# Optimization experiments

Hardware: AMD Instinct MI355X
Metric: run time of the kernel (lower is better)

Reference implementation:

```python
import jax, jax.numpy as jnp
import numpy as np

B, DIM, COND, HID = 500000, 3, 64, 128
IN = DIM + COND + 1  # z + context + time feature


def setup_inputs() -> dict:
    key = jax.random.key(0)
    ks = jax.random.split(key, 8)
    s_in = 1.0 / np.sqrt(IN)
    s_h = 1.0 / np.sqrt(HID)
    return {
        "t": jnp.float32(0.5),
        "z": jax.random.normal(ks[0], (B, DIM), jnp.float32),
        "logp": jnp.zeros((B, 1), jnp.float32),
        "context": jax.random.normal(ks[1], (B, COND), jnp.float32),
        "eps": jax.random.normal(ks[2], (B, DIM), jnp.float32),
        "W_in": jax.random.normal(ks[3], (IN, HID), jnp.float32) * s_in,
        "b_in": jnp.zeros((HID,), jnp.float32),
        "W_h1": jax.random.normal(ks[4], (HID, HID), jnp.float32) * s_h,
        "b_h1": jnp.zeros((HID,), jnp.float32),
        "W_h2": jax.random.normal(ks[5], (HID, HID), jnp.float32) * s_h,
        "b_h2": jnp.zeros((HID,), jnp.float32),
        "W_out": jax.random.normal(ks[6], (HID, DIM), jnp.float32) * s_h,
        "b_out": jnp.zeros((DIM,), jnp.float32),
        "out_scale": jnp.float32(1.0),
    }


def reference(t, z, logp, context, eps, W_in, b_in, W_h1, b_h1, W_h2, b_h2,
              W_out, b_out, out_scale):
    t_feat = jnp.full((z.shape[0], 1), t, dtype=z.dtype)

    def vel(zz):
        inp = jnp.concatenate([zz, context, t_feat], axis=1)  # (B, IN)
        h = jnp.tanh(inp @ W_in + b_in)
        h = jnp.tanh(h @ W_h1 + b_h1)
        h = jnp.tanh(h @ W_h2 + b_h2)
        return (h @ W_out + b_out) * out_scale  # (B, DIM)

    # Hutchinson trace: tr(df/dz) ~= eps^T (d/dz)(f . eps) via vjp with cotangent eps
    f, vjp_fn = jax.vjp(vel, z)
    (gz,) = vjp_fn(eps)
    neg_div = -jnp.sum(gz * eps, axis=1, keepdims=True)  # (B, 1)
    return f, neg_div
```

## Files before the change

kernel.cpp:

```cpp
#include <hip/hip_runtime.h>


#define B_N    500000
#define NT32   15625
#define GRID   256
#define NSTR   (GRID * 8)

#define L_WFIN   0
#define L_WF1    8704
#define L_WF2    25600
#define L_WB2    42496
#define L_WB1    59392
#define L_WOUTP  76288
#define L_WOUTT  76800
#define L_WIN3   77196
#define L_F16END 77592
#define N_BIAS   384
#define PREP_N   (L_F16END + N_BIAS)
#define BIAS_BYTE   155184
#define OUTST_BYTE  156720
#define LDS_BYTES   159792
#define COPY16      9795

typedef _Float16 f16x4 __attribute__((ext_vector_type(4)));
typedef float    f32x4 __attribute__((ext_vector_type(4)));

union U4 { f16x4 v; _Float16 e[4]; uint2 d; };

static __device__ inline f16x4 lds_a4(const _Float16* p) {
    U4 u; u.d = *reinterpret_cast<const uint2*>(p); return u.v;
}

#define MFMA(a, b, c) __builtin_amdgcn_mfma_f32_16x16x16f16((a), (b), (c), 0, 0, 0)

static __device__ inline float ftanh(float x) {
    float e = __expf(2.f * x);
    return 1.f - 2.f * __builtin_amdgcn_rcpf(e + 1.f);
}

__global__ void prep_kernel(const float* __restrict__ W_in,
                            const float* __restrict__ W_h1,
                            const float* __restrict__ W_h2,
                            const float* __restrict__ W_out,
                            const float* __restrict__ b_in,
                            const float* __restrict__ b_h1,
                            const float* __restrict__ b_h2,
                            _Float16* __restrict__ ws) {
    int i = blockIdx.x * 256 + threadIdx.x;
    if (i >= PREP_N) return;
    if (i >= L_F16END) {
        int bi = i - L_F16END;
        float* bp = reinterpret_cast<float*>(ws + L_F16END);
        bp[bi] = (bi < 128) ? b_in[bi] : (bi < 256) ? b_h1[bi - 128]
                                                    : b_h2[bi - 256];
        return;
    }
    float v = 0.f;
    if (i < L_WF1) {
        int n = i / 68, k = i - n * 68;
        if      (k < 64)  v = W_in[(3 + k) * 128 + n];
        else if (k < 67)  v = W_in[(k - 64) * 128 + n];
        else              v = W_in[67 * 128 + n];
    } else if (i < L_WF2) {
        int j = i - L_WF1; int n = j / 132, a = j - n * 132;
        if (a < 128) v = W_h1[a * 128 + n];
    } else if (i < L_WB2) {
        int j = i - L_WF2; int n = j / 132, a = j - n * 132;
        if (a < 128) v = W_h2[a * 128 + n];
    } else if (i < L_WB1) {
        int j = i - L_WB2; int r = j / 132, b = j - r * 132;
        if (b < 128) v = W_h2[r * 128 + b];
    } else if (i < L_WOUTP) {
        int j = i - L_WB1; int r = j / 132, b = j - r * 132;
        if (b < 128) v = W_h1[r * 128 + b];
    } else if (i < L_WOUTT) {
        int j = i - L_WOUTP; int n = j >> 2, k = j & 3;
        if (k < 3) v = W_out[n * 3 + k];
    } else if (i < L_WIN3) {
        int j = i - L_WOUTT; int d = j / 132, n = j - d * 132;
        if (n < 128) v = W_out[n * 3 + d];
    } else {
        int j = i - L_WIN3; int d = j / 132, a = j - d * 132;
        if (a < 128) v = W_in[d * 128 + a];
    }
    ws[i] = (_Float16)v;
}

__global__ __launch_bounds__(512, 1) void fused_kernel(
        const float* __restrict__ t_p,  const float* __restrict__ z,
        const float* __restrict__ ctx,  const float* __restrict__ eps,
        const float* __restrict__ b_out, const float* __restrict__ os_p,
        const _Float16* __restrict__ ws, float* __restrict__ out) {
    extern __shared__ _Float16 smem[];
    const int tid  = threadIdx.x;
    const int wave = tid >> 6;
    const int lane = tid & 63;
    const int l15  = lane & 15;
    const int q    = lane >> 4;

    {
        const uint4* src = reinterpret_cast<const uint4*>(ws);
        uint4* dst = reinterpret_cast<uint4*>(smem);
        for (int i = tid; i < COPY16; i += 512) dst[i] = src[i];
    }
    __syncthreads();

    const _Float16* WFIN  = smem + L_WFIN;
    const _Float16* WF1   = smem + L_WF1;
    const _Float16* WF2   = smem + L_WF2;
    const _Float16* WB2   = smem + L_WB2;
    const _Float16* WB1   = smem + L_WB1;
    const _Float16* WOUTP = smem + L_WOUTP;
    const _Float16* WOUTT = smem + L_WOUTT;
    const _Float16* WIN3  = smem + L_WIN3;
    const float* biasf =
        reinterpret_cast<const float*>(reinterpret_cast<char*>(smem) + BIAS_BYTE);
    float* outst =
        reinterpret_cast<float*>(reinterpret_cast<char*>(smem) + OUTST_BYTE)
        + wave * 96;

    const float tval = t_p[0];
    const float os   = os_p[0];
    const float bo0 = b_out[0], bo1 = b_out[1], bo2 = b_out[2];
    float* out_f  = out;
    float* out_nd = out + (size_t)B_N * 3;

    const f32x4 zero4 = {0.f, 0.f, 0.f, 0.f};

    for (int t = blockIdx.x * 8 + wave; t < NT32; t += NSTR) {
        const int gb = t * 32;

        U4 epsb[2];
        float ee[2][3];
        #pragma unroll
        for (int c = 0; c < 2; ++c) {
            epsb[c].d.x = 0u; epsb[c].d.y = 0u;
            ee[c][0] = ee[c][1] = ee[c][2] = 0.f;
            if (q == 0) {
                const float* ep = eps + (size_t)(gb + 16 * c + l15) * 3;
                ee[c][0] = ep[0]; ee[c][1] = ep[1]; ee[c][2] = ep[2];
                epsb[c].e[0] = (_Float16)ee[c][0];
                epsb[c].e[1] = (_Float16)ee[c][1];
                epsb[c].e[2] = (_Float16)ee[c][2];
            }
        }

        f32x4 acc[8][2];
        #pragma unroll
        for (int m = 0; m < 8; ++m) { acc[m][0] = zero4; acc[m][1] = zero4; }

        #pragma unroll
        for (int kk = 0; kk < 4; ++kk) {
            U4 b[2];
            #pragma unroll
            for (int c = 0; c < 2; ++c) {
                const float4 cv = *reinterpret_cast<const float4*>(
                    ctx + (size_t)(gb + 16 * c + l15) * 64 + kk * 16 + 4 * q);
                b[c].e[0] = (_Float16)cv.x; b[c].e[1] = (_Float16)cv.y;
                b[c].e[2] = (_Float16)cv.z; b[c].e[3] = (_Float16)cv.w;
            }
            #pragma unroll
            for (int m = 0; m < 8; ++m) {
                f16x4 a = lds_a4(WFIN + (16 * m + l15) * 68 + kk * 16 + 4 * q);
                acc[m][0] = MFMA(a, b[0].v, acc[m][0]);
                acc[m][1] = MFMA(a, b[1].v, acc[m][1]);
            }
        }
        {
            U4 b[2];
            #pragma unroll
            for (int c = 0; c < 2; ++c) {
                b[c].d.x = 0u; b[c].d.y = 0u;
                if (q == 0) {
                    const float* zp = z + (size_t)(gb + 16 * c + l15) * 3;
                    b[c].e[0] = (_Float16)zp[0]; b[c].e[1] = (_Float16)zp[1];
                    b[c].e[2] = (_Float16)zp[2]; b[c].e[3] = (_Float16)tval;
                }
            }
            #pragma unroll
            for (int m = 0; m < 8; ++m) {
                f16x4 a = lds_a4(WFIN + (16 * m + l15) * 68 + 64 + 4 * q);
                acc[m][0] = MFMA(a, b[0].v, acc[m][0]);
                acc[m][1] = MFMA(a, b[1].v, acc[m][1]);
            }
        }
        U4 h1p[8][2];
        #pragma unroll
        for (int m = 0; m < 8; ++m) {
            const float4 bb = *reinterpret_cast<const float4*>(
                biasf + 0 + 16 * m + 4 * q);
            #pragma unroll
            for (int c = 0; c < 2; ++c) {
                h1p[m][c].e[0] = (_Float16)ftanh(acc[m][c][0] + bb.x);
                h1p[m][c].e[1] = (_Float16)ftanh(acc[m][c][1] + bb.y);
                h1p[m][c].e[2] = (_Float16)ftanh(acc[m][c][2] + bb.z);
                h1p[m][c].e[3] = (_Float16)ftanh(acc[m][c][3] + bb.w);
            }
        }

        #pragma unroll
        for (int m = 0; m < 8; ++m) { acc[m][0] = zero4; acc[m][1] = zero4; }
        #pragma unroll
        for (int kk = 0; kk < 8; ++kk) {
            #pragma unroll
            for (int m = 0; m < 8; ++m) {
                f16x4 a = lds_a4(WF1 + (16 * m + l15) * 132 + 16 * kk + 4 * q);
                acc[m][0] = MFMA(a, h1p[kk][0].v, acc[m][0]);
                acc[m][1] = MFMA(a, h1p[kk][1].v, acc[m][1]);
            }
        }
        U4 h2p[8][2];
        #pragma unroll
        for (int m = 0; m < 8; ++m) {
            const float4 bb = *reinterpret_cast<const float4*>(
                biasf + 128 + 16 * m + 4 * q);
            #pragma unroll
            for (int c = 0; c < 2; ++c) {
                h2p[m][c].e[0] = (_Float16)ftanh(acc[m][c][0] + bb.x);
                h2p[m][c].e[1] = (_Float16)ftanh(acc[m][c][1] + bb.y);
                h2p[m][c].e[2] = (_Float16)ftanh(acc[m][c][2] + bb.z);
                h2p[m][c].e[3] = (_Float16)ftanh(acc[m][c][3] + bb.w);
            }
        }

        #pragma unroll
        for (int m = 0; m < 8; ++m) { acc[m][0] = zero4; acc[m][1] = zero4; }
        #pragma unroll
        for (int kk = 0; kk < 8; ++kk) {
            #pragma unroll
            for (int m = 0; m < 8; ++m) {
                f16x4 a = lds_a4(WF2 + (16 * m + l15) * 132 + 16 * kk + 4 * q);
                acc[m][0] = MFMA(a, h2p[kk][0].v, acc[m][0]);
                acc[m][1] = MFMA(a, h2p[kk][1].v, acc[m][1]);
            }
        }
        U4 h3p[8][2], u3p[8][2];
        #pragma unroll
        for (int m = 0; m < 8; ++m) {
            const float4 bb = *reinterpret_cast<const float4*>(
                biasf + 256 + 16 * m + 4 * q);
            f16x4 a3 = lds_a4(WOUTP + (16 * m + l15) * 4 + 4 * q);
            #pragma unroll
            for (int c = 0; c < 2; ++c) {
                f32x4 up = MFMA(a3, epsb[c].v, zero4);
                #pragma unroll
                for (int i = 0; i < 4; ++i) {
                    float bi = (i == 0) ? bb.x : (i == 1) ? bb.y
                              : (i == 2) ? bb.z : bb.w;
                    float h = ftanh(acc[m][c][i] + bi);
                    h3p[m][c].e[i] = (_Float16)h;
                    u3p[m][c].e[i] = (_Float16)(os * up[i] * (1.f - h * h));
                }
            }
        }

        {
            f32x4 f0 = zero4, f1 = zero4;
            #pragma unroll
            for (int kk = 0; kk < 8; ++kk) {
                f16x4 a = lds_a4(WOUTT + l15 * 132 + 16 * kk + 4 * q);
                f0 = MFMA(a, h3p[kk][0].v, f0);
                f1 = MFMA(a, h3p[kk][1].v, f1);
            }
            if (q == 0) {
                outst[(0 * 16 + l15) * 3 + 0] = (f0[0] + bo0) * os;
                outst[(0 * 16 + l15) * 3 + 1] = (f0[1] + bo1) * os;
                outst[(0 * 16 + l15) * 3 + 2] = (f0[2] + bo2) * os;
                outst[(1 * 16 + l15) * 3 + 0] = (f1[0] + bo0) * os;
                outst[(1 * 16 + l15) * 3 + 1] = (f1[1] + bo1) * os;
                outst[(1 * 16 + l15) * 3 + 2] = (f1[2] + bo2) * os;
            }
        }

        #pragma unroll
        for (int m = 0; m < 8; ++m) { acc[m][0] = zero4; acc[m][1] = zero4; }
        #pragma unroll
        for (int kk = 0; kk < 8; ++kk) {
            #pragma unroll
            for (int m = 0; m < 8; ++m) {
                f16x4 a = lds_a4(WB2 + (16 * m + l15) * 132 + 16 * kk + 4 * q);
                acc[m][0] = MFMA(a, u3p[kk][0].v, acc[m][0]);
                acc[m][1] = MFMA(a, u3p[kk][1].v, acc[m][1]);
            }
        }
        #pragma unroll
        for (int m = 0; m < 8; ++m)
            #pragma unroll
            for (int c = 0; c < 2; ++c) {
                U4 u2;
                #pragma unroll
                for (int i = 0; i < 4; ++i) {
                    float h = (float)h2p[m][c].e[i];
                    u2.e[i] = (_Float16)(acc[m][c][i] * (1.f - h * h));
                }
                h2p[m][c] = u2;
            }

        #pragma unroll
        for (int m = 0; m < 8; ++m) { acc[m][0] = zero4; acc[m][1] = zero4; }
        #pragma unroll
        for (int kk = 0; kk < 8; ++kk) {
            #pragma unroll
            for (int m = 0; m < 8; ++m) {
                f16x4 a = lds_a4(WB1 + (16 * m + l15) * 132 + 16 * kk + 4 * q);
                acc[m][0] = MFMA(a, h2p[kk][0].v, acc[m][0]);
                acc[m][1] = MFMA(a, h2p[kk][1].v, acc[m][1]);
            }
        }
        #pragma unroll
        for (int m = 0; m < 8; ++m)
            #pragma unroll
            for (int c = 0; c < 2; ++c) {
                U4 u1;
                #pragma unroll
                for (int i = 0; i < 4; ++i) {
                    float h = (float)h1p[m][c].e[i];
                    u1.e[i] = (_Float16)(acc[m][c][i] * (1.f - h * h));
                }
                h1p[m][c] = u1;
            }

        {
            f32x4 g0 = zero4, g1 = zero4;
            #pragma unroll
            for (int kk = 0; kk < 8; ++kk) {
                f16x4 a = lds_a4(WIN3 + l15 * 132 + 16 * kk + 4 * q);
                g0 = MFMA(a, h1p[kk][0].v, g0);
                g1 = MFMA(a, h1p[kk][1].v, g1);
            }
            if (q == 0) {
                out_nd[gb + l15] =
                    -(g0[0] * ee[0][0] + g0[1] * ee[0][1] + g0[2] * ee[0][2]);
                out_nd[gb + 16 + l15] =
                    -(g1[0] * ee[1][0] + g1[1] * ee[1][1] + g1[2] * ee[1][2]);
            }
        }

        if (lane < 24) {
            float4 v = *reinterpret_cast<const float4*>(outst + lane * 4);
            *reinterpret_cast<float4*>(out_f + (size_t)gb * 3 + lane * 4) = v;
        }
    }
}

extern "C" void kernel_launch(void* const* d_in, const int* in_sizes, int n_in,
                              void* d_out, int out_size, void* d_ws, size_t ws_size,
                              hipStream_t stream) {
    const float* t_p   = (const float*)d_in[0];
    const float* z     = (const float*)d_in[1];
    const float* ctx   = (const float*)d_in[3];
    const float* eps   = (const float*)d_in[4];
    const float* W_in  = (const float*)d_in[5];
    const float* b_in  = (const float*)d_in[6];
    const float* W_h1  = (const float*)d_in[7];
    const float* b_h1  = (const float*)d_in[8];
    const float* W_h2  = (const float*)d_in[9];
    const float* b_h2  = (const float*)d_in[10];
    const float* W_out = (const float*)d_in[11];
    const float* b_out = (const float*)d_in[12];
    const float* os_p  = (const float*)d_in[13];
    _Float16* ws = (_Float16*)d_ws;
    float* out = (float*)d_out;

    static bool attr_set = false;
    if (!attr_set) {
        (void)hipFuncSetAttribute((const void*)fused_kernel,
                                  hipFuncAttributeMaxDynamicSharedMemorySize,
                                  LDS_BYTES);
        attr_set = true;
    }

    prep_kernel<<<(PREP_N + 255) / 256, 256, 0, stream>>>(
        W_in, W_h1, W_h2, W_out, b_in, b_h1, b_h2, ws);
    fused_kernel<<<GRID, 512, LDS_BYTES, stream>>>(
        t_p, z, ctx, eps, b_out, os_p, ws, out);
}
```

Baseline: 334.8 us.

## Switch to 16x16x32 MFMA with permuted weights and raise to 12 waves per block

After: 356.0 us. 1.06x slower.

```diff
diff --git a/kernel.cpp b/kernel.cpp
--- a/kernel.cpp
+++ b/kernel.cpp
@@ -4,7 +4,8 @@
 #define B_N    500000
 #define NT32   15625
 #define GRID   256
-#define NSTR   (GRID * 8)
+#define WPB    12
+#define NSTR   (GRID * WPB)
 
 #define L_WFIN   0
 #define L_WF1    8704
@@ -19,23 +20,36 @@
 #define PREP_N   (L_F16END + N_BIAS)
 #define BIAS_BYTE   155184
 #define OUTST_BYTE  156720
-#define LDS_BYTES   159792
+#define LDS_BYTES   161328
 #define COPY16      9795
 
 typedef _Float16 f16x4 __attribute__((ext_vector_type(4)));
+typedef _Float16 f16x8 __attribute__((ext_vector_type(8)));
 typedef float    f32x4 __attribute__((ext_vector_type(4)));
 
 union U4 { f16x4 v; _Float16 e[4]; uint2 d; };
+union U8 { f16x8 v; f16x4 h[2]; _Float16 e[8]; uint2 d2[2]; };
 
 static __device__ inline f16x4 lds_a4(const _Float16* p) {
     U4 u; u.d = *reinterpret_cast<const uint2*>(p); return u.v;
 }
-
-#define MFMA(a, b, c) __builtin_amdgcn_mfma_f32_16x16x16f16((a), (b), (c), 0, 0, 0)
+static __device__ inline f16x8 lds_a8(const _Float16* p) {
+    U8 u;
+    u.d2[0] = *reinterpret_cast<const uint2*>(p);
+    u.d2[1] = *reinterpret_cast<const uint2*>(p + 4);
+    return u.v;
+}
+
+#define MFMA16(a, b, c) __builtin_amdgcn_mfma_f32_16x16x16f16((a), (b), (c), 0, 0, 0)
+#define MFMA32(a, b, c) __builtin_amdgcn_mfma_f32_16x16x32_f16((a), (b), (c), 0, 0, 0)
 
 static __device__ inline float ftanh(float x) {
     float e = __expf(2.f * x);
     return 1.f - 2.f * __builtin_amdgcn_rcpf(e + 1.f);
+}
+
+static __device__ inline int sig(int p) {
+    return (p & ~31) | ((p & 4) << 2) | ((p >> 1) & 12) | (p & 3);
 }
 
 __global__ void prep_kernel(const float* __restrict__ W_in,
@@ -63,30 +77,30 @@
         else              v = W_in[67 * 128 + n];
     } else if (i < L_WF2) {
         int j = i - L_WF1; int n = j / 132, a = j - n * 132;
-        if (a < 128) v = W_h1[a * 128 + n];
+        if (a < 128) v = W_h1[sig(a) * 128 + n];
     } else if (i < L_WB2) {
         int j = i - L_WF2; int n = j / 132, a = j - n * 132;
-        if (a < 128) v = W_h2[a * 128 + n];
+        if (a < 128) v = W_h2[sig(a) * 128 + n];
     } else if (i < L_WB1) {
         int j = i - L_WB2; int r = j / 132, b = j - r * 132;
-        if (b < 128) v = W_h2[r * 128 + b];
+        if (b < 128) v = W_h2[r * 128 + sig(b)];
     } else if (i < L_WOUTP) {
         int j = i - L_WB1; int r = j / 132, b = j - r * 132;
-        if (b < 128) v = W_h1[r * 128 + b];
+        if (b < 128) v = W_h1[r * 128 + sig(b)];
     } else if (i < L_WOUTT) {
         int j = i - L_WOUTP; int n = j >> 2, k = j & 3;
         if (k < 3) v = W_out[n * 3 + k];
     } else if (i < L_WIN3) {
         int j = i - L_WOUTT; int d = j / 132, n = j - d * 132;
-        if (n < 128) v = W_out[n * 3 + d];
+        if (n < 128) v = W_out[sig(n) * 3 + d];
     } else {
         int j = i - L_WIN3; int d = j / 132, a = j - d * 132;
-        if (a < 128) v = W_in[d * 128 + a];
+        if (a < 128) v = W_in[d * 128 + sig(a)];
     }
     ws[i] = (_Float16)v;
 }
 
-__global__ __launch_bounds__(512, 1) void fused_kernel(
+__global__ __launch_bounds__(768, 3) void fused_kernel(
         const float* __restrict__ t_p,  const float* __restrict__ z,
         const float* __restrict__ ctx,  const float* __restrict__ eps,
         const float* __restrict__ b_out, const float* __restrict__ os_p,
@@ -101,7 +115,7 @@
     {
         const uint4* src = reinterpret_cast<const uint4*>(ws);
         uint4* dst = reinterpret_cast<uint4*>(smem);
-        for (int i = tid; i < COPY16; i += 512) dst[i] = src[i];
+        for (int i = tid; i < COPY16; i += 768) dst[i] = src[i];
     }
     __syncthreads();
 
@@ -127,7 +141,7 @@
 
     const f32x4 zero4 = {0.f, 0.f, 0.f, 0.f};
 
-    for (int t = blockIdx.x * 8 + wave; t < NT32; t += NSTR) {
+    for (int t = blockIdx.x + wave * GRID; t < NT32; t += NSTR) {
         const int gb = t * 32;
 
         U4 epsb[2];
@@ -145,195 +159,183 @@
             }
         }
 
-        f32x4 acc[8][2];
-        #pragma unroll
-        for (int m = 0; m < 8; ++m) { acc[m][0] = zero4; acc[m][1] = zero4; }
-
-        #pragma unroll
-        for (int kk = 0; kk < 4; ++kk) {
-            U4 b[2];
+        U8 cb[2][2];
+        #pragma unroll
+        for (int a = 0; a < 2; ++a)
             #pragma unroll
             for (int c = 0; c < 2; ++c) {
-                const float4 cv = *reinterpret_cast<const float4*>(
-                    ctx + (size_t)(gb + 16 * c + l15) * 64 + kk * 16 + 4 * q);
-                b[c].e[0] = (_Float16)cv.x; b[c].e[1] = (_Float16)cv.y;
-                b[c].e[2] = (_Float16)cv.z; b[c].e[3] = (_Float16)cv.w;
-            }
-            #pragma unroll
-            for (int m = 0; m < 8; ++m) {
-                f16x4 a = lds_a4(WFIN + (16 * m + l15) * 68 + kk * 16 + 4 * q);
-                acc[m][0] = MFMA(a, b[0].v, acc[m][0]);
-                acc[m][1] = MFMA(a, b[1].v, acc[m][1]);
-            }
-        }
-        {
-            U4 b[2];
-            #pragma unroll
-            for (int c = 0; c < 2; ++c) {
-                b[c].d.x = 0u; b[c].d.y = 0u;
-                if (q == 0) {
-                    const float* zp = z + (size_t)(gb + 16 * c + l15) * 3;
-                    b[c].e[0] = (_Float16)zp[0]; b[c].e[1] = (_Float16)zp[1];
-                    b[c].e[2] = (_Float16)zp[2]; b[c].e[3] = (_Float16)tval;
-                }
-            }
-            #pragma unroll
-            for (int m = 0; m < 8; ++m) {
-                f16x4 a = lds_a4(WFIN + (16 * m + l15) * 68 + 64 + 4 * q);
-                acc[m][0] = MFMA(a, b[0].v, acc[m][0]);
-                acc[m][1] = MFMA(a, b[1].v, acc[m][1]);
-            }
-        }
-        U4 h1p[8][2];
+                const float* cp = ctx + (size_t)(gb + 16 * c + l15) * 64
+                                  + a * 32 + 8 * q;
+                const float4 v0 = *reinterpret_cast<const float4*>(cp);
+                const float4 v1 = *reinterpret_cast<const float4*>(cp + 4);
+                cb[a][c].e[0] = (_Float16)v0.x; cb[a][c].e[1] = (_Float16)v0.y;
+                cb[a][c].e[2] = (_Float16)v0.z; cb[a][c].e[3] = (_Float16)v0.w;
+                cb[a][c].e[4] = (_Float16)v1.x; cb[a][c].e[5] = (_Float16)v1.y;
+                cb[a][c].e[6] = (_Float16)v1.z; cb[a][c].e[7] = (_Float16)v1.w;
+            }
+        U4 bz[2];
+        #pragma unroll
+        for (int c = 0; c < 2; ++c) {
+            bz[c].d.x = 0u; bz[c].d.y = 0u;
+            if (q == 0) {
+                const float* zp = z + (size_t)(gb + 16 * c + l15) * 3;
+                bz[c].e[0] = (_Float16)zp[0]; bz[c].e[1] = (_Float16)zp[1];
+                bz[c].e[2] = (_Float16)zp[2]; bz[c].e[3] = (_Float16)tval;
+            }
+        }
+
+        U8 h1p[4][2];
         #pragma unroll
         for (int m = 0; m < 8; ++m) {
+            f32x4 a0 = zero4, a1 = zero4;
+            #pragma unroll
+            for (int a = 0; a < 2; ++a) {
+                f16x8 A = lds_a8(WFIN + (16 * m + l15) * 68 + a * 32 + 8 * q);
+                a0 = MFMA32(A, cb[a][0].v, a0);
+                a1 = MFMA32(A, cb[a][1].v, a1);
+            }
+            {
+                f16x4 A4 = lds_a4(WFIN + (16 * m + l15) * 68 + 64 + 4 * q);
+                a0 = MFMA16(A4, bz[0].v, a0);
+                a1 = MFMA16(A4, bz[1].v, a1);
+            }
             const float4 bb = *reinterpret_cast<const float4*>(
                 biasf + 0 + 16 * m + 4 * q);
             #pragma unroll
             for (int c = 0; c < 2; ++c) {
-                h1p[m][c].e[0] = (_Float16)ftanh(acc[m][c][0] + bb.x);
-                h1p[m][c].e[1] = (_Float16)ftanh(acc[m][c][1] + bb.y);
-                h1p[m][c].e[2] = (_Float16)ftanh(acc[m][c][2] + bb.z);
-                h1p[m][c].e[3] = (_Float16)ftanh(acc[m][c][3] + bb.w);
-            }
-        }
-
-        #pragma unroll
-        for (int m = 0; m < 8; ++m) { acc[m][0] = zero4; acc[m][1] = zero4; }
-        #pragma unroll
-        for (int kk = 0; kk < 8; ++kk) {
-            #pragma unroll
-            for (int m = 0; m < 8; ++m) {
-                f16x4 a = lds_a4(WF1 + (16 * m + l15) * 132 + 16 * kk + 4 * q);
-                acc[m][0] = MFMA(a, h1p[kk][0].v, acc[m][0]);
-                acc[m][1] = MFMA(a, h1p[kk][1].v, acc[m][1]);
-            }
-        }
-        U4 h2p[8][2];
+                const f32x4 ac = c ? a1 : a0;
+                h1p[m >> 1][c].e[(m & 1) * 4 + 0] = (_Float16)ftanh(ac[0] + bb.x);
+                h1p[m >> 1][c].e[(m & 1) * 4 + 1] = (_Float16)ftanh(ac[1] + bb.y);
+                h1p[m >> 1][c].e[(m & 1) * 4 + 2] = (_Float16)ftanh(ac[2] + bb.z);
+                h1p[m >> 1][c].e[(m & 1) * 4 + 3] = (_Float16)ftanh(ac[3] + bb.w);
+            }
+        }
+
+        U8 h2p[4][2];
         #pragma unroll
         for (int m = 0; m < 8; ++m) {
+            f32x4 a0 = zero4, a1 = zero4;
+            #pragma unroll
+            for (int a = 0; a < 4; ++a) {
+                f16x8 A = lds_a8(WF1 + (16 * m + l15) * 132 + a * 32 + 8 * q);
+                a0 = MFMA32(A, h1p[a][0].v, a0);
+                a1 = MFMA32(A, h1p[a][1].v, a1);
+            }
             const float4 bb = *reinterpret_cast<const float4*>(
                 biasf + 128 + 16 * m + 4 * q);
             #pragma unroll
             for (int c = 0; c < 2; ++c) {
-                h2p[m][c].e[0] = (_Float16)ftanh(acc[m][c][0] + bb.x);
-                h2p[m][c].e[1] = (_Float16)ftanh(acc[m][c][1] + bb.y);
-                h2p[m][c].e[2] = (_Float16)ftanh(acc[m][c][2] + bb.z);
-                h2p[m][c].e[3] = (_Float16)ftanh(acc[m][c][3] + bb.w);
-            }
-        }
-
-        #pragma unroll
-        for (int m = 0; m < 8; ++m) { acc[m][0] = zero4; acc[m][1] = zero4; }
-        #pragma unroll
-        for (int kk = 0; kk < 8; ++kk) {
-            #pragma unroll
-            for (int m = 0; m < 8; ++m) {
-                f16x4 a = lds_a4(WF2 + (16 * m + l15) * 132 + 16 * kk + 4 * q);
-                acc[m][0] = MFMA(a, h2p[kk][0].v, acc[m][0]);
-                acc[m][1] = MFMA(a, h2p[kk][1].v, acc[m][1]);
-            }
-        }
-        U4 h3p[8][2], u3p[8][2];
+                const f32x4 ac = c ? a1 : a0;
+                h2p[m >> 1][c].e[(m & 1) * 4 + 0] = (_Float16)ftanh(ac[0] + bb.x);
+                h2p[m >> 1][c].e[(m & 1) * 4 + 1] = (_Float16)ftanh(ac[1] + bb.y);
+                h2p[m >> 1][c].e[(m & 1) * 4 + 2] = (_Float16)ftanh(ac[2] + bb.z);
+                h2p[m >> 1][c].e[(m & 1) * 4 + 3] = (_Float16)ftanh(ac[3] + bb.w);
+            }
+        }
+
+        U8 u3p[4][2];
+        f32x4 f0 = zero4, f1 = zero4;
+        #pragma unroll
+        for (int mp = 0; mp < 4; ++mp) {
+            U8 h3pr[2];
+            #pragma unroll
+            for (int sub = 0; sub < 2; ++sub) {
+                const int m = 2 * mp + sub;
+                f32x4 a0 = zero4, a1 = zero4;
+                #pragma unroll
+                for (int a = 0; a < 4; ++a) {
+                    f16x8 A = lds_a8(WF2 + (16 * m + l15) * 132 + a * 32 + 8 * q);
+                    a0 = MFMA32(A, h2p[a][0].v, a0);
+                    a1 = MFMA32(A, h2p[a][1].v, a1);
+                }
+                f16x4 a3 = lds_a4(WOUTP + (16 * m + l15) * 4 + 4 * q);
+                f32x4 up0 = MFMA16(a3, epsb[0].v, zero4);
+                f32x4 up1 = MFMA16(a3, epsb[1].v, zero4);
+                const float4 bb = *reinterpret_cast<const float4*>(
+                    biasf + 256 + 16 * m + 4 * q);
+                #pragma unroll
+                for (int c = 0; c < 2; ++c) {
+                    const f32x4 ac = c ? a1 : a0;
+                    const f32x4 uc = c ? up1 : up0;
+                    #pragma unroll
+                    for (int i = 0; i < 4; ++i) {
+                        float bi = (i == 0) ? bb.x : (i == 1) ? bb.y
+                                  : (i == 2) ? bb.z : bb.w;
+                        float h = ftanh(ac[i] + bi);
+                        h3pr[c].e[sub * 4 + i] = (_Float16)h;
+                        u3p[mp][c].e[sub * 4 + i] =
+                            (_Float16)(os * uc[i] * (1.f - h * h));
+                    }
+                }
+            }
+            f16x8 Af = lds_a8(WOUTT + l15 * 132 + mp * 32 + 8 * q);
+            f0 = MFMA32(Af, h3pr[0].v, f0);
+            f1 = MFMA32(Af, h3pr[1].v, f1);
+        }
+        if (q == 0) {
+            outst[(0 * 16 + l15) * 3 + 0] = (f0[0] + bo0) * os;
+            outst[(0 * 16 + l15) * 3 + 1] = (f0[1] + bo1) * os;
+            outst[(0 * 16 + l15) * 3 + 2] = (f0[2] + bo2) * os;
+            outst[(1 * 16 + l15) * 3 + 0] = (f1[0] + bo0) * os;
+            outst[(1 * 16 + l15) * 3 + 1] = (f1[1] + bo1) * os;
+            outst[(1 * 16 + l15) * 3 + 2] = (f1[2] + bo2) * os;
+        }
+
         #pragma unroll
         for (int m = 0; m < 8; ++m) {
-            const float4 bb = *reinterpret_cast<const float4*>(
-                biasf + 256 + 16 * m + 4 * q);
-            f16x4 a3 = lds_a4(WOUTP + (16 * m + l15) * 4 + 4 * q);
+            f32x4 a0 = zero4, a1 = zero4;
+            #pragma unroll
+            for (int a = 0; a < 4; ++a) {
+                f16x8 A = lds_a8(WB2 + (16 * m + l15) * 132 + a * 32 + 8 * q);
+                a0 = MFMA32(A, u3p[a][0].v, a0);
+                a1 = MFMA32(A, u3p[a][1].v, a1);
+            }
             #pragma unroll
             for (int c = 0; c < 2; ++c) {
-                f32x4 up = MFMA(a3, epsb[c].v, zero4);
+                const f32x4 ac = c ? a1 : a0;
                 #pragma unroll
                 for (int i = 0; i < 4; ++i) {
-                    float bi = (i == 0) ? bb.x : (i == 1) ? bb.y
-                              : (i == 2) ? bb.z : bb.w;
-                    float h = ftanh(acc[m][c][i] + bi);
-                    h3p[m][c].e[i] = (_Float16)h;
-                    u3p[m][c].e[i] = (_Float16)(os * up[i] * (1.f - h * h));
-                }
-            }
-        }
-
-        {
-            f32x4 f0 = zero4, f1 = zero4;
-            #pragma unroll
-            for (int kk = 0; kk < 8; ++kk) {
-                f16x4 a = lds_a4(WOUTT + l15 * 132 + 16 * kk + 4 * q);
-                f0 = MFMA(a, h3p[kk][0].v, f0);
-                f1 = MFMA(a, h3p[kk][1].v, f1);
-            }
-            if (q == 0) {
-                outst[(0 * 16 + l15) * 3 + 0] = (f0[0] + bo0) * os;
-                outst[(0 * 16 + l15) * 3 + 1] = (f0[1] + bo1) * os;
-                outst[(0 * 16 + l15) * 3 + 2] = (f0[2] + bo2) * os;
-                outst[(1 * 16 + l15) * 3 + 0] = (f1[0] + bo0) * os;
-                outst[(1 * 16 + l15) * 3 + 1] = (f1[1] + bo1) * os;
-                outst[(1 * 16 + l15) * 3 + 2] = (f1[2] + bo2) * os;
-            }
-        }
-
-        #pragma unroll
-        for (int m = 0; m < 8; ++m) { acc[m][0] = zero4; acc[m][1] = zero4; }
-        #pragma unroll
-        for (int kk = 0; kk < 8; ++kk) {
-            #pragma unroll
-            for (int m = 0; m < 8; ++m) {
-                f16x4 a = lds_a4(WB2 + (16 * m + l15) * 132 + 16 * kk + 4 * q);
-                acc[m][0] = MFMA(a, u3p[kk][0].v, acc[m][0]);
-                acc[m][1] = MFMA(a, u3p[kk][1].v, acc[m][1]);
-            }
-        }
-        #pragma unroll
-        for (int m = 0; m < 8; ++m)
-            #pragma unroll
-            for (int c = 0; c < 2; ++c) {
-                U4 u2;
-                #pragma unroll
-                for (int i = 0; i < 4; ++i) {
-                    float h = (float)h2p[m][c].e[i];
-                    u2.e[i] = (_Float16)(acc[m][c][i] * (1.f - h * h));
-                }
-                h2p[m][c] = u2;
-            }
-
-        #pragma unroll
-        for (int m = 0; m < 8; ++m) { acc[m][0] = zero4; acc[m][1] = zero4; }
-        #pragma unroll
-        for (int kk = 0; kk < 8; ++kk) {
-            #pragma unroll
-            for (int m = 0; m < 8; ++m) {
-                f16x4 a = lds_a4(WB1 + (16 * m + l15) * 132 + 16 * kk + 4 * q);
-                acc[m][0] = MFMA(a, h2p[kk][0].v, acc[m][0]);
-                acc[m][1] = MFMA(a, h2p[kk][1].v, acc[m][1]);
-            }
-        }
-        #pragma unroll
-        for (int m = 0; m < 8; ++m)
-            #pragma unroll
-            for (int c = 0; c < 2; ++c) {
-                U4 u1;
-                #pragma unroll
-                for (int i = 0; i < 4; ++i) {
-                    float h = (float)h1p[m][c].e[i];
-                    u1.e[i] = (_Float16)(acc[m][c][i] * (1.f - h * h));
-                }
-                h1p[m][c] = u1;
-            }
-
-        {
-            f32x4 g0 = zero4, g1 = zero4;
-            #pragma unroll
-            for (int kk = 0; kk < 8; ++kk) {
-                f16x4 a = lds_a4(WIN3 + l15 * 132 + 16 * kk + 4 * q);
-                g0 = MFMA(a, h1p[kk][0].v, g0);
-                g1 = MFMA(a, h1p[kk][1].v, g1);
-            }
-            if (q == 0) {
-                out_nd[gb + l15] =
-                    -(g0[0] * ee[0][0] + g0[1] * ee[0][1] + g0[2] * ee[0][2]);
-                out_nd[gb + 16 + l15] =
-                    -(g1[0] * ee[1][0] + g1[1] * ee[1][1] + g1[2] * ee[1][2]);
-            }
+                    float h = (float)h2p[m >> 1][c].e[(m & 1) * 4 + i];
+                    h2p[m >> 1][c].e[(m & 1) * 4 + i] =
+                        (_Float16)(ac[i] * (1.f - h * h));
+                }
+            }
+        }
+
+        f32x4 g0 = zero4, g1 = zero4;
+        #pragma unroll
+        for (int mp = 0; mp < 4; ++mp) {
+            U8 u1pr[2];
+            #pragma unroll
+            for (int sub = 0; sub < 2; ++sub) {
+                const int m = 2 * mp + sub;
+                f32x4 a0 = zero4, a1 = zero4;
+                #pragma unroll
+                for (int a = 0; a < 4; ++a) {
+                    f16x8 A = lds_a8(WB1 + (16 * m + l15) * 132 + a * 32 + 8 * q);
+                    a0 = MFMA32(A, h2p[a][0].v, a0);
+                    a1 = MFMA32(A, h2p[a][1].v, a1);
+                }
+                #pragma unroll
+                for (int c = 0; c < 2; ++c) {
+                    const f32x4 ac = c ? a1 : a0;
+                    #pragma unroll
+                    for (int i = 0; i < 4; ++i) {
+                        float h = (float)h1p[m >> 1][c].e[(m & 1) * 4 + i];
+                        u1pr[c].e[sub * 4 + i] =
+                            (_Float16)(ac[i] * (1.f - h * h));
+                    }
+                }
+            }
+            f16x8 Ag = lds_a8(WIN3 + l15 * 132 + mp * 32 + 8 * q);
+            g0 = MFMA32(Ag, u1pr[0].v, g0);
+            g1 = MFMA32(Ag, u1pr[1].v, g1);
+        }
+        if (q == 0) {
+            out_nd[gb + l15] =
+                -(g0[0] * ee[0][0] + g0[1] * ee[0][1] + g0[2] * ee[0][2]);
+            out_nd[gb + 16 + l15] =
+                -(g1[0] * ee[1][0] + g1[1] * ee[1][1] + g1[2] * ee[1][2]);
         }
 
         if (lane < 24) {
@@ -372,6 +374,6 @@
 
     prep_kernel<<<(PREP_N + 255) / 256, 256, 0, stream>>>(
         W_in, W_h1, W_h2, W_out, b_in, b_h1, b_h2, ws);
-    fused_kernel<<<GRID, 512, LDS_BYTES, stream>>>(
+    fused_kernel<<<GRID, 768, LDS_BYTES, stream>>>(
         t_p, z, ctx, eps, b_out, os_p, ws, out);
 }
```
